# Kernel tuning notes

Measured on AMD Instinct MI355X. Metric: run time of the kernel, lower is better.

The kernel has to match this reference:

```python
import jax, jax.numpy as jnp
import numpy as np

B, T, E, H = 4, 2048, 1024, 16
HD = E // H

def setup_inputs() -> dict:
    key = jax.random.key(0)
    ks = jax.random.split(key, 5)
    s = 1.0 / np.sqrt(E)
    return {
        "x": jax.random.normal(ks[0], (B, T, E), dtype=jnp.float32),
        "mask": jnp.zeros((B, T), dtype=bool),
        "qkv_w": jax.random.uniform(ks[1], (3 * E, E), jnp.float32, -s, s),
        "qkv_b": jax.random.uniform(ks[2], (3 * E,), jnp.float32, -s, s),
        "proj_w": jax.random.uniform(ks[3], (E, E), jnp.float32, -s, s),
        "proj_b": jax.random.uniform(ks[4], (E,), jnp.float32, -s, s),
    }

def reference(x, mask, qkv_w, qkv_b, proj_w, proj_b):
    b, t, e = x.shape
    qkv = x @ qkv_w.T + qkv_b                      # [b,t,3e]
    q, k, v = jnp.split(qkv, 3, axis=2)
    # [b,t,e] -> [b,h,t,hd]
    q = q.reshape(b, t, H, HD).transpose(0, 2, 1, 3)
    k = k.reshape(b, t, H, HD).transpose(0, 2, 1, 3)
    v = v.reshape(b, t, H, HD).transpose(0, 2, 1, 3)
    scale = 1.0 / np.sqrt(HD)
    attn = jnp.einsum('bhqd,bhkd->bhqk', q, k) * scale
    # mask: True -> -inf, broadcast over heads and query positions
    neg = jnp.where(mask, -jnp.inf, 0.0).astype(attn.dtype)  # [b,t]
    attn = attn + neg[:, None, None, :]
    attn = jax.nn.softmax(attn, axis=-1)
    # dropout layers in eval mode (deterministic reference)
    out = jnp.einsum('bhqk,bhkd->bhqd', attn, v)   # [b,h,t,hd]
    out = out.transpose(0, 2, 1, 3).reshape(b, t, e)
    return out @ proj_w.T + proj_b
```

## Files before the change

kernel.cpp:

```cpp
#include <hip/hip_runtime.h>
#include <stdint.h>

#define Bz  4
#define Tz  2048
#define Ez  1024
#define Hz  16
#define HDz 64
#define Mz  (Bz*Tz)

typedef short bf16x8 __attribute__((ext_vector_type(8)));
typedef float f32x4  __attribute__((ext_vector_type(4)));
typedef unsigned short u16;

__device__ __forceinline__ u16 f2bf(float f) {
  return (u16)((__builtin_bit_cast(uint32_t, f) + 0x8000u) >> 16);
}
__device__ __forceinline__ uint32_t pack2bf(float a, float b) {
  uint32_t ua = __builtin_bit_cast(uint32_t, a) + 0x8000u;
  uint32_t ub = __builtin_bit_cast(uint32_t, b) + 0x8000u;
  return __builtin_amdgcn_perm(ub, ua, 0x07060302u);
}
__device__ __forceinline__ uint32_t cvtpk2bf(float a, float b) {
  uint32_t r;
  asm("v_cvt_pk_bf16_f32 %0, %1, %2" : "=v"(r) : "v"(a), "v"(b));
  return r;
}

#if __has_builtin(__builtin_amdgcn_exp2f)
#define EXP2(x) __builtin_amdgcn_exp2f(x)
#else
#define EXP2(x) exp2f(x)
#endif

__device__ __forceinline__ void gl2lds16(const u16* g, u16* l) {
  __builtin_amdgcn_global_load_lds((const __attribute__((address_space(1))) void*)g,
                                   (__attribute__((address_space(3))) void*)l, 16, 0, 0);
}

__global__ void cvt_f32_bf16_3(const float* __restrict__ s0, u16* __restrict__ d0, int n0,
                               const float* __restrict__ s1, u16* __restrict__ d1, int n1,
                               const float* __restrict__ s2, u16* __restrict__ d2, int n2) {
  int j = blockIdx.x * blockDim.x + threadIdx.x;
  const float* s; u16* d;
  if (j < n0) { s = s0; d = d0; }
  else {
    j -= n0;
    if (j < n1) { s = s1; d = d1; }
    else { j -= n1; if (j >= n2) return; s = s2; d = d2; }
  }
  float4 f = ((const float4*)s)[j];
  uint2 o;
  o.x = pack2bf(f.x, f.y);
  o.y = pack2bf(f.z, f.w);
  ((uint2*)d)[j] = o;
}

template<int MODE>
__global__ __launch_bounds__(512, 2) void gemm_bt(
    const u16* __restrict__ A, const u16* __restrict__ Bw,
    const float* __restrict__ bias,
    u16* __restrict__ qo, u16* __restrict__ ko, u16* __restrict__ vto,
    float* __restrict__ fo)
{
  __shared__ u16 Lds[3][(256 + 128) * 64];
  const int tid  = threadIdx.x;
  const int lane = tid & 63;
  const int wid  = tid >> 6;
  const int quad = lane >> 4;
  const int cl   = lane & 15;
  const int wm   = wid >> 1;
  const int wn   = wid & 1;
  const int bm   = blockIdx.y * 256;
  const int bn   = blockIdx.x * 128;
  const int srow8 = lane >> 3;
  const int sch   = lane & 7;

  f32x4 acc[4][4] = {};

  auto stage = [&](int t, int buf) {
    const int kt = t * 64;
    u16* base = &Lds[buf][0];
#pragma unroll
    for (int s = 0; s < 4; ++s) {
      const int r  = s*64 + wid*8 + srow8;
      const int cc = sch ^ (r & 7);
      gl2lds16(A + (size_t)(bm + r)*Ez + kt + cc*8, base + (s*64 + wid*8)*64);
    }
#pragma unroll
    for (int s = 0; s < 2; ++s) {
      const int r  = s*64 + wid*8 + srow8;
      const int cc = sch ^ (r & 7);
      gl2lds16(Bw + (size_t)(bn + r)*Ez + kt + cc*8, base + (256*64) + (s*64 + wid*8)*64);
    }
  };

  stage(0, 0);
  stage(1, 1);

#pragma unroll
  for (int t = 0; t < 16; ++t) {
    const int buf = t % 3;
    if (t + 2 < 16) stage(t + 2, (t + 2) % 3);
    if (t < 14)       asm volatile("s_waitcnt vmcnt(12)" ::: "memory");
    else if (t == 14) asm volatile("s_waitcnt vmcnt(6)"  ::: "memory");
    else              asm volatile("s_waitcnt vmcnt(0)"  ::: "memory");
    __builtin_amdgcn_s_barrier();
    __builtin_amdgcn_sched_barrier(0);
    const u16* AB = &Lds[buf][0];
    const u16* BB = &Lds[buf][256*64];
#pragma unroll
    for (int ks = 0; ks < 2; ++ks) {
      bf16x8 af[4], bfr[4];
#pragma unroll
      for (int mi = 0; mi < 4; ++mi) {
        const int row = wm*64 + mi*16 + cl;
        const int ch  = (ks*4 + quad) ^ (row & 7);
        af[mi] = *(const bf16x8*)&AB[row*64 + ch*8];
      }
#pragma unroll
      for (int ni = 0; ni < 4; ++ni) {
        const int row = wn*64 + ni*16 + cl;
        const int ch  = (ks*4 + quad) ^ (row & 7);
        bfr[ni] = *(const bf16x8*)&BB[row*64 + ch*8];
      }
      __builtin_amdgcn_s_setprio(1);
#pragma unroll
      for (int mi = 0; mi < 4; ++mi)
#pragma unroll
        for (int ni = 0; ni < 4; ++ni)
          acc[mi][ni] = __builtin_amdgcn_mfma_f32_16x16x32_bf16(af[mi], bfr[ni], acc[mi][ni], 0, 0, 0);
      __builtin_amdgcn_s_setprio(0);
    }
    __builtin_amdgcn_s_barrier();
  }

  const float qsc = 0.125f * 1.4426950408889634f;
#pragma unroll
  for (int ni = 0; ni < 4; ++ni) {
    const int n   = bn + wn*64 + ni*16 + cl;
    const float bv = bias[n];
#pragma unroll
    for (int mi = 0; mi < 4; ++mi) {
      const int m0 = bm + wm*64 + mi*16 + quad*4;
      if (MODE == 0) {
        const int which = n >> 10;
        const int e = n & 1023;
        const int h = e >> 6, d = e & 63;
        const int b = m0 >> 11, t0 = m0 & 2047;
        if (which == 2) {
          uint2 pk;
          pk.x = pack2bf(acc[mi][ni][0] + bv, acc[mi][ni][1] + bv);
          pk.y = pack2bf(acc[mi][ni][2] + bv, acc[mi][ni][3] + bv);
          *(uint2*)&vto[(((size_t)(b*Hz + h))*HDz + d)*Tz + t0] = pk;
        } else {
#pragma unroll
          for (int r = 0; r < 4; ++r) {
            const int t = t0 + r;
            float val = acc[mi][ni][r] + bv;
            if (which == 0) qo[(((size_t)(b*Hz + h))*Tz + t)*HDz + d] = f2bf(val * qsc);
            else            ko[(((size_t)(b*Hz + h))*Tz + t)*HDz + d] = f2bf(val);
          }
        }
      } else {
#pragma unroll
        for (int r = 0; r < 4; ++r)
          fo[(size_t)(m0 + r)*Ez + n] = acc[mi][ni][r] + bv;
      }
    }
  }
}

__global__ __launch_bounds__(256, 4) void attn_flash(
    const u16* __restrict__ Q, const u16* __restrict__ K,
    const u16* __restrict__ Vt, const unsigned char* __restrict__ mask,
    u16* __restrict__ ctx)
{
  __shared__ u16 Kb[2][64*64];
  __shared__ u16 Vb[2][64*64];

  const int tid  = threadIdx.x;
  const int lane = tid & 63;
  const int wid  = tid >> 6;
  const int quad = lane >> 4;
  const int cl   = lane & 15;
  const int bh   = blockIdx.x;
  const int b    = bh >> 4;
  const int qrw  = blockIdx.y * 128 + wid * 32;

  const int srow = wid*16 + (lane >> 3);
  const int sch  = (lane & 7) ^ (srow & 7);
  const u16* Kg = K  + ((size_t)bh*Tz + srow)*HDz + sch*8;
  const u16* Vg = Vt + ((size_t)bh*HDz + srow)*Tz + sch*8;
  u16* KbL[2] = { &Kb[0][(wid*16)*64], &Kb[1][(wid*16)*64] };
  u16* VbL[2] = { &Vb[0][(wid*16)*64], &Vb[1][(wid*16)*64] };

  auto stage = [&](int kt, int buf) {
    gl2lds16(Kg + (size_t)kt*HDz,           KbL[buf]);
    gl2lds16(Kg + (size_t)kt*HDz + 8*HDz,   KbL[buf] + 8*64);
    gl2lds16(Vg + kt,                       VbL[buf]);
    gl2lds16(Vg + kt + (size_t)8*Tz,        VbL[buf] + 8*64);
  };

  const unsigned char* mrow_p = mask + (size_t)b * Tz;
  bool domask;
  {
    const uint4* mp = (const uint4*)mrow_p;
    uint4 a = mp[lane*2], c = mp[lane*2 + 1];
    uint32_t any = a.x | a.y | a.z | a.w | c.x | c.y | c.z | c.w;
    domask = __any(any != 0);
  }

  bf16x8 aq[2][2];
#pragma unroll
  for (int qb = 0; qb < 2; ++qb) {
    const u16* Qg = Q + ((size_t)bh*Tz + qrw + qb*16 + cl)*HDz;
    aq[qb][0] = *(const bf16x8*)(Qg + quad*8);
    aq[qb][1] = *(const bf16x8*)(Qg + 32 + quad*8);
  }

  bf16x8 ones;
#pragma unroll
  for (int i = 0; i < 8; ++i) ones[i] = (short)0x3F80;

  f32x4 o[2][4] = {};
  f32x4 lacc[2] = {};

  stage(0, 0);

#pragma unroll 2
  for (int it = 0; it < 32; ++it) {
    const int bufc = it & 1;
    __syncthreads();
    if (it < 31) stage((it+1)*64, bufc^1);
    const u16* KB = &Kb[bufc][0];
    const u16* VB = &Vb[bufc][0];
    const int kt = it * 64;

#pragma unroll
    for (int kv = 0; kv < 2; ++kv) {
      f32x4 st[2][2] = {};
#pragma unroll
      for (int kb = 0; kb < 2; ++kb) {
        bf16x8 kf[2];
#pragma unroll
        for (int nb = 0; nb < 2; ++nb) {
          const int row = kv*32 + nb*16 + cl;
          const int ch  = (kb*4 + quad) ^ (row & 7);
          kf[nb] = *(const bf16x8*)&KB[row*64 + ch*8];
        }
#pragma unroll
        for (int qb = 0; qb < 2; ++qb)
#pragma unroll
          for (int nb = 0; nb < 2; ++nb)
            st[qb][nb] = __builtin_amdgcn_mfma_f32_16x16x32_bf16(kf[nb], aq[qb][kb], st[qb][nb], 0, 0, 0);
      }

      if (domask) {
#pragma unroll
        for (int nb = 0; nb < 2; ++nb) {
          uint32_t mm = *(const uint32_t*)&mrow_p[kt + kv*32 + nb*16 + quad*4];
          if (mm) {
#pragma unroll
            for (int qb = 0; qb < 2; ++qb) {
              if (mm & 0x000000ffu) st[qb][nb][0] = -INFINITY;
              if (mm & 0x0000ff00u) st[qb][nb][1] = -INFINITY;
              if (mm & 0x00ff0000u) st[qb][nb][2] = -INFINITY;
              if (mm & 0xff000000u) st[qb][nb][3] = -INFINITY;
            }
          }
        }
      }

      bf16x8 pf[2];
#pragma unroll
      for (int qb = 0; qb < 2; ++qb) {
        uint32_t ux = cvtpk2bf(EXP2(st[qb][0][0]), EXP2(st[qb][0][1]));
        uint32_t uy = cvtpk2bf(EXP2(st[qb][0][2]), EXP2(st[qb][0][3]));
        uint32_t vx = cvtpk2bf(EXP2(st[qb][1][0]), EXP2(st[qb][1][1]));
        uint32_t vy = cvtpk2bf(EXP2(st[qb][1][2]), EXP2(st[qb][1][3]));
        asm("v_permlane32_swap_b32 %0, %1" : "+v"(ux), "+v"(vx));
        asm("v_permlane32_swap_b32 %0, %1" : "+v"(uy), "+v"(vy));
        asm("v_permlane16_swap_b32 %0, %1" : "+v"(ux), "+v"(vx));
        asm("v_permlane16_swap_b32 %0, %1" : "+v"(uy), "+v"(vy));
        int4 pi = { (int)ux, (int)uy, (int)vx, (int)vy };
        pf[qb] = __builtin_bit_cast(bf16x8, pi);
        lacc[qb] = __builtin_amdgcn_mfma_f32_16x16x32_bf16(pf[qb], ones, lacc[qb], 0, 0, 0);
      }

#pragma unroll
      for (int db = 0; db < 4; ++db) {
        const int row = db*16 + cl;
        const int ch  = (kv*4 + quad) ^ (row & 7);
        bf16x8 bv = *(const bf16x8*)&VB[row*64 + ch*8];
#pragma unroll
        for (int qb = 0; qb < 2; ++qb)
          o[qb][db] = __builtin_amdgcn_mfma_f32_16x16x32_bf16(pf[qb], bv, o[qb][db], 0, 0, 0);
      }
    }
  }

#pragma unroll
  for (int qb = 0; qb < 2; ++qb) {
#pragma unroll
    for (int r = 0; r < 4; ++r) {
      const float inv = 1.0f / lacc[qb][r];
      const int t = qrw + qb*16 + quad*4 + r;
      const size_t base = ((size_t)b*Tz + t)*Ez + (size_t)(bh & 15)*HDz;
#pragma unroll
      for (int db = 0; db < 4; ++db) {
        ctx[base + db*16 + cl] = f2bf(o[qb][db][r] * inv);
      }
    }
  }
}

extern "C" void kernel_launch(void* const* d_in, const int* in_sizes, int n_in,
                              void* d_out, int out_size, void* d_ws, size_t ws_size,
                              hipStream_t stream) {
  (void)in_sizes; (void)n_in; (void)out_size; (void)ws_size;
  const float* x      = (const float*)d_in[0];
  const unsigned char* mask = (const unsigned char*)d_in[1];
  const float* qkv_w  = (const float*)d_in[2];
  const float* qkv_b  = (const float*)d_in[3];
  const float* proj_w = (const float*)d_in[4];
  const float* proj_b = (const float*)d_in[5];
  float* out = (float*)d_out;

  char* ws = (char*)d_ws;
  u16* xb   = (u16*)(ws + 0);
  u16* wqb  = (u16*)(ws + 16777216);
  u16* wpb  = (u16*)(ws + 23068672);
  u16* Qb   = (u16*)(ws + 25165824);
  u16* Kb_  = (u16*)(ws + 41943040);
  u16* Vtb  = (u16*)(ws + 58720256);
  u16* ctxb = (u16*)(ws + 75497472);

  cvt_f32_bf16_3<<<12288, 256, 0, stream>>>(x, xb, 2097152,
                                            qkv_w, wqb, 786432,
                                            proj_w, wpb, 262144);

  gemm_bt<0><<<dim3(24, 32), 512, 0, stream>>>(xb, wqb, qkv_b, Qb, Kb_, Vtb, nullptr);
  attn_flash<<<dim3(64, 16), 256, 0, stream>>>(Qb, Kb_, Vtb, mask, ctxb);
  gemm_bt<1><<<dim3(8, 32), 512, 0, stream>>>(ctxb, wpb, proj_b, nullptr, nullptr, nullptr, out);
}
```

Measured before the change: 253.9 us.

## Restructure GEMM tile to 128x256 and interleave staged loads with MFMA phases

Changes the GEMM block tile from 256x128 to 128x256 with a 2x4 wave grid and adjusts launch grids to match. The main loop is split into four sub-phases, each loading fragments and issuing a slice of the next global-to-LDS stage before its MFMA group. This spreads memory traffic across the compute to improve overlap. The cost is more barriers per iteration and a changed waitcnt accounting that must stay correct.

New measurement: 263.5 us. 1.04x slower.

```diff
diff --git a/kernel.cpp b/kernel.cpp
--- a/kernel.cpp
+++ b/kernel.cpp
@@ -62,76 +62,118 @@
     u16* __restrict__ qo, u16* __restrict__ ko, u16* __restrict__ vto,
     float* __restrict__ fo)
 {
-  __shared__ u16 Lds[3][(256 + 128) * 64];
+  __shared__ u16 Lds[3][(128 + 256) * 64];
   const int tid  = threadIdx.x;
   const int lane = tid & 63;
   const int wid  = tid >> 6;
   const int quad = lane >> 4;
   const int cl   = lane & 15;
-  const int wm   = wid >> 1;
-  const int wn   = wid & 1;
-  const int bm   = blockIdx.y * 256;
-  const int bn   = blockIdx.x * 128;
-  const int srow8 = lane >> 3;
-  const int sch   = lane & 7;
+  const int wm   = wid >> 2;
+  const int wn   = wid & 3;
+  const int bm   = blockIdx.y * 128;
+  const int bn   = blockIdx.x * 256;
+
+  const int srow = tid >> 3;
+  const int scc  = (tid & 7) ^ (srow & 7);
+  const u16* Ag = A  + (size_t)(bm + srow)*Ez + scc*8;
+  const u16* Bg = Bw + (size_t)(bn + srow)*Ez + scc*8;
 
   f32x4 acc[4][4] = {};
 
-  auto stage = [&](int t, int buf) {
-    const int kt = t * 64;
-    u16* base = &Lds[buf][0];
-#pragma unroll
-    for (int s = 0; s < 4; ++s) {
-      const int r  = s*64 + wid*8 + srow8;
-      const int cc = sch ^ (r & 7);
-      gl2lds16(A + (size_t)(bm + r)*Ez + kt + cc*8, base + (s*64 + wid*8)*64);
-    }
-#pragma unroll
-    for (int s = 0; s < 2; ++s) {
-      const int r  = s*64 + wid*8 + srow8;
-      const int cc = sch ^ (r & 7);
-      gl2lds16(Bw + (size_t)(bn + r)*Ez + kt + cc*8, base + (256*64) + (s*64 + wid*8)*64);
-    }
+  auto stA = [&](int slot, int j, int kt) {
+    gl2lds16(Ag + (size_t)(j*64)*Ez + kt, &Lds[slot][j*4096 + tid*8]);
   };
-
-  stage(0, 0);
-  stage(1, 1);
+  auto stB = [&](int slot, int j, int kt) {
+    gl2lds16(Bg + (size_t)(j*64)*Ez + kt, &Lds[slot][128*64 + j*4096 + tid*8]);
+  };
+
+  stB(0,0,0);  stB(0,1,0);  stB(0,2,0);  stB(0,3,0);  stA(0,0,0);  stA(0,1,0);
+  stB(1,0,64); stB(1,1,64); stB(1,2,64); stB(1,3,64); stA(1,0,64); stA(1,1,64);
+  asm volatile("s_waitcnt vmcnt(6)" ::: "memory");
+  __builtin_amdgcn_s_barrier();
+
+  const int ch0 = quad ^ (cl & 7);
+  const int ch1 = (4 + quad) ^ (cl & 7);
 
 #pragma unroll
   for (int t = 0; t < 16; ++t) {
-    const int buf = t % 3;
-    if (t + 2 < 16) stage(t + 2, (t + 2) % 3);
-    if (t < 14)       asm volatile("s_waitcnt vmcnt(12)" ::: "memory");
-    else if (t == 14) asm volatile("s_waitcnt vmcnt(6)"  ::: "memory");
-    else              asm volatile("s_waitcnt vmcnt(0)"  ::: "memory");
+    const int slot = t % 3;
+    const int s2   = (t + 2) % 3;
+    const int kt2  = (t + 2) * 64;
+    const bool st  = (t + 2) < 16;
+    const u16* AB = &Lds[slot][0];
+    const u16* BB = &Lds[slot][128*64];
+
+    bf16x8 af[2], bfr[4];
+
+#pragma unroll
+    for (int i = 0; i < 2; ++i)
+      af[i] = *(const bf16x8*)&AB[(wm*64 + i*16 + cl)*64 + ch0*8];
+#pragma unroll
+    for (int n = 0; n < 4; ++n)
+      bfr[n] = *(const bf16x8*)&BB[(wn*64 + n*16 + cl)*64 + ch0*8];
+    if (st) { stB(s2,0,kt2); stB(s2,1,kt2); }
     __builtin_amdgcn_s_barrier();
+    asm volatile("s_waitcnt lgkmcnt(0)" ::: "memory");
     __builtin_amdgcn_sched_barrier(0);
-    const u16* AB = &Lds[buf][0];
-    const u16* BB = &Lds[buf][256*64];
-#pragma unroll
-    for (int ks = 0; ks < 2; ++ks) {
-      bf16x8 af[4], bfr[4];
-#pragma unroll
-      for (int mi = 0; mi < 4; ++mi) {
-        const int row = wm*64 + mi*16 + cl;
-        const int ch  = (ks*4 + quad) ^ (row & 7);
-        af[mi] = *(const bf16x8*)&AB[row*64 + ch*8];
-      }
-#pragma unroll
-      for (int ni = 0; ni < 4; ++ni) {
-        const int row = wn*64 + ni*16 + cl;
-        const int ch  = (ks*4 + quad) ^ (row & 7);
-        bfr[ni] = *(const bf16x8*)&BB[row*64 + ch*8];
-      }
-      __builtin_amdgcn_s_setprio(1);
-#pragma unroll
-      for (int mi = 0; mi < 4; ++mi)
-#pragma unroll
-        for (int ni = 0; ni < 4; ++ni)
-          acc[mi][ni] = __builtin_amdgcn_mfma_f32_16x16x32_bf16(af[mi], bfr[ni], acc[mi][ni], 0, 0, 0);
-      __builtin_amdgcn_s_setprio(0);
-    }
+    __builtin_amdgcn_s_setprio(1);
+#pragma unroll
+    for (int i = 0; i < 2; ++i)
+#pragma unroll
+      for (int n = 0; n < 4; ++n)
+        acc[i][n] = __builtin_amdgcn_mfma_f32_16x16x32_bf16(af[i], bfr[n], acc[i][n], 0, 0, 0);
+    __builtin_amdgcn_s_setprio(0);
+
+#pragma unroll
+    for (int i = 0; i < 2; ++i)
+      af[i] = *(const bf16x8*)&AB[(wm*64 + (2+i)*16 + cl)*64 + ch0*8];
+    if (st) { stB(s2,2,kt2); stB(s2,3,kt2); }
     __builtin_amdgcn_s_barrier();
+    asm volatile("s_waitcnt lgkmcnt(0)" ::: "memory");
+    __builtin_amdgcn_sched_barrier(0);
+    __builtin_amdgcn_s_setprio(1);
+#pragma unroll
+    for (int i = 0; i < 2; ++i)
+#pragma unroll
+      for (int n = 0; n < 4; ++n)
+        acc[2+i][n] = __builtin_amdgcn_mfma_f32_16x16x32_bf16(af[i], bfr[n], acc[2+i][n], 0, 0, 0);
+    __builtin_amdgcn_s_setprio(0);
+
+#pragma unroll
+    for (int i = 0; i < 2; ++i)
+      af[i] = *(const bf16x8*)&AB[(wm*64 + i*16 + cl)*64 + ch1*8];
+#pragma unroll
+    for (int n = 0; n < 4; ++n)
+      bfr[n] = *(const bf16x8*)&BB[(wn*64 + n*16 + cl)*64 + ch1*8];
+    if (st) { stA(s2,0,kt2); stA(s2,1,kt2); }
+    __builtin_amdgcn_s_barrier();
+    asm volatile("s_waitcnt lgkmcnt(0)" ::: "memory");
+    __builtin_amdgcn_sched_barrier(0);
+    __builtin_amdgcn_s_setprio(1);
+#pragma unroll
+    for (int i = 0; i < 2; ++i)
+#pragma unroll
+      for (int n = 0; n < 4; ++n)
+        acc[i][n] = __builtin_amdgcn_mfma_f32_16x16x32_bf16(af[i], bfr[n], acc[i][n], 0, 0, 0);
+    __builtin_amdgcn_s_setprio(0);
+
+#pragma unroll
+    for (int i = 0; i < 2; ++i)
+      af[i] = *(const bf16x8*)&AB[(wm*64 + (2+i)*16 + cl)*64 + ch1*8];
+    __builtin_amdgcn_s_barrier();
+    asm volatile("s_waitcnt lgkmcnt(0)" ::: "memory");
+    __builtin_amdgcn_sched_barrier(0);
+    __builtin_amdgcn_s_setprio(1);
+#pragma unroll
+    for (int i = 0; i < 2; ++i)
+#pragma unroll
+      for (int n = 0; n < 4; ++n)
+        acc[2+i][n] = __builtin_amdgcn_mfma_f32_16x16x32_bf16(af[i], bfr[n], acc[2+i][n], 0, 0, 0);
+    __builtin_amdgcn_s_setprio(0);
+
+    if (t < 14)       asm volatile("s_waitcnt vmcnt(6)" ::: "memory");
+    else if (t == 14) asm volatile("s_waitcnt vmcnt(0)" ::: "memory");
+    if (t < 15) __builtin_amdgcn_s_barrier();
   }
 
   const float qsc = 0.125f * 1.4426950408889634f;
@@ -339,7 +381,7 @@
                                             qkv_w, wqb, 786432,
                                             proj_w, wpb, 262144);
 
-  gemm_bt<0><<<dim3(24, 32), 512, 0, stream>>>(xb, wqb, qkv_b, Qb, Kb_, Vtb, nullptr);
+  gemm_bt<0><<<dim3(12, 64), 512, 0, stream>>>(xb, wqb, qkv_b, Qb, Kb_, Vtb, nullptr);
   attn_flash<<<dim3(64, 16), 256, 0, stream>>>(Qb, Kb_, Vtb, mask, ctxb);
-  gemm_bt<1><<<dim3(8, 32), 512, 0, stream>>>(ctxb, wpb, proj_b, nullptr, nullptr, nullptr, out);
-}
+  gemm_bt<1><<<dim3(4, 64), 512, 0, stream>>>(ctxb, wpb, proj_b, nullptr, nullptr, nullptr, out);
+}
```
